# Kernel optimization log

Hardware: AMD Instinct MI355X
Metric: run time of the kernel (lower is better)

## Reference

```python
import jax, jax.numpy as jnp
import numpy as np

D_MODEL = 768
N_HEADS = 12
D_HEAD = D_MODEL // N_HEADS

def setup_inputs() -> dict:
    key = jax.random.key(0)
    ks = jax.random.split(key, 5)
    B, T = 2, 4096
    x = jax.random.normal(ks[0], (B, T, D_MODEL), dtype=jnp.float32)
    s_in = 1.0 / np.sqrt(D_MODEL)
    W_qkv = jax.random.normal(ks[1], (D_MODEL, 3 * D_MODEL), dtype=jnp.float32) * s_in
    b_qkv = jnp.zeros((3 * D_MODEL,), dtype=jnp.float32)
    W_proj = jax.random.normal(ks[2], (D_MODEL, D_MODEL), dtype=jnp.float32) * s_in
    b_proj = jnp.zeros((D_MODEL,), dtype=jnp.float32)
    return {"x": x, "W_qkv": W_qkv, "b_qkv": b_qkv, "W_proj": W_proj, "b_proj": b_proj}

def reference(x, W_qkv, b_qkv, W_proj, b_proj):
    B, T, C = x.shape
    qkv = x @ W_qkv + b_qkv                      # [B,T,3C]
    q, k, v = jnp.split(qkv, 3, axis=-1)
    def heads(t):
        return t.reshape(B, T, N_HEADS, D_HEAD).transpose(0, 2, 1, 3)  # [B,H,T,d]
    q, k, v = heads(q), heads(k), heads(v)
    scale = 1.0 / np.sqrt(D_HEAD)
    att = jnp.einsum('bhqd,bhkd->bhqk', q, k) * scale  # [B,H,T,T]
    causal = jnp.tril(jnp.ones((T, T), dtype=bool))
    att = jnp.where(causal[None, None], att, -jnp.inf)
    att = jax.nn.softmax(att, axis=-1)
    y = jnp.einsum('bhqk,bhkd->bhqd', att, v)          # [B,H,T,d]
    y = y.transpose(0, 2, 1, 3).reshape(B, T, C)
    return y @ W_proj + b_proj
```

## Files before the change

### kernel.cpp

```cpp
#include <hip/hip_runtime.h>
#include <hip/hip_bf16.h>

typedef __bf16 bf16_t;
typedef bf16_t bf16x8 __attribute__((ext_vector_type(8)));
typedef float  f32x4  __attribute__((ext_vector_type(4)));

#define TSEQ   4096
#define NBATCH 2
#define DMODEL 768
#define NHEADS 12
#define DHEAD  64
#define NTOK   (NBATCH*TSEQ)
#define NQKV   (3*DMODEL)

#define QSCALE 0.18033688011112042f
#define SMAX 24.0f

__device__ __forceinline__ f32x4 mfma16(bf16x8 a, bf16x8 b, f32x4 c) {
  return __builtin_amdgcn_mfma_f32_16x16x32_bf16(a, b, c, 0, 0, 0);
}

__device__ __forceinline__ void glds16(const bf16_t* g, bf16_t* l) {
  __builtin_amdgcn_global_load_lds(
      (const __attribute__((address_space(1))) void*)g,
      (__attribute__((address_space(3))) void*)l, 16, 0, 0);
}

__global__ void k_cvt(const float* __restrict__ in, bf16_t* __restrict__ out, int n) {
  int i = blockIdx.x * blockDim.x + threadIdx.x;
  if (i < n) out[i] = (bf16_t)in[i];
}

__global__ __launch_bounds__(256) void k_transpose_cvt(
    const float* __restrict__ in, bf16_t* __restrict__ out, int R, int C) {
  __shared__ bf16_t tile[64][66];
  const int c0 = blockIdx.x * 64, r0 = blockIdx.y * 64;
  const int tid = threadIdx.x;
  const int r = tid >> 2, cb = (tid & 3) * 16;
  const float* ip = in + (long)(r0 + r) * C + c0 + cb;
#pragma unroll
  for (int k = 0; k < 16; k += 4) {
    float4 v = *(const float4*)(ip + k);
    tile[r][cb + k + 0] = (bf16_t)v.x;
    tile[r][cb + k + 1] = (bf16_t)v.y;
    tile[r][cb + k + 2] = (bf16_t)v.z;
    tile[r][cb + k + 3] = (bf16_t)v.w;
  }
  __syncthreads();
  const int c = tid >> 2, rb = (tid & 3) * 16;
  bf16_t* op = out + (long)(c0 + c) * R + r0 + rb;
  bf16x8 v0, v1;
#pragma unroll
  for (int i = 0; i < 8; ++i) { v0[i] = tile[rb + i][c]; v1[i] = tile[rb + 8 + i][c]; }
  *(bf16x8*)(op) = v0;
  *(bf16x8*)(op + 8) = v1;
}

__device__ __forceinline__ void gemm_core(
    const bf16_t* __restrict__ A, const bf16_t* __restrict__ Bt,
    int m0, int n0, bf16_t* As, bf16_t* Bs, f32x4 acc[2][8]) {
  const int tid  = threadIdx.x;
  const int wave = tid >> 6;
  const int lane = tid & 63;
  const int quad = lane >> 4;
  const int l16  = lane & 15;
  const int srow = lane >> 2;
  const int scol = (lane & 3) * 8;

  const bf16_t* a0 = A + (long)(m0 + wave * 16 + srow) * DMODEL + scol;
  const bf16_t* b0 = Bt + (long)(n0 + wave * 16 + srow) * DMODEL + scol;

  glds16(a0,               As + wave * 16 * 32);
  glds16(a0 + 64 * DMODEL, As + (64 + wave * 16) * 32);
  glds16(b0,               Bs + wave * 16 * 32);
  glds16(b0 + 64 * DMODEL, Bs + (64 + wave * 16) * 32);
  __syncthreads();

  for (int ks = 0; ks < DMODEL / 32; ++ks) {
    const int p = ks & 1;
    if (ks + 1 < DMODEL / 32) {
      const int k1 = (ks + 1) * 32;
      bf16_t* Asx = (p ? As : As + 128 * 32);
      bf16_t* Bsx = (p ? Bs : Bs + 128 * 32);
      glds16(a0 + k1,               Asx + wave * 16 * 32);
      glds16(a0 + 64 * DMODEL + k1, Asx + (64 + wave * 16) * 32);
      glds16(b0 + k1,               Bsx + wave * 16 * 32);
      glds16(b0 + 64 * DMODEL + k1, Bsx + (64 + wave * 16) * 32);
    }
    const bf16_t* Ap = As + p * (128 * 32);
    const bf16_t* Bp = Bs + p * (128 * 32);

    bf16x8 af0 = *(const bf16x8*)(Ap + (wave * 32 + l16) * 32 + quad * 8);
    bf16x8 af1 = *(const bf16x8*)(Ap + (wave * 32 + 16 + l16) * 32 + quad * 8);
#pragma unroll
    for (int nt = 0; nt < 8; ++nt) {
      bf16x8 bfm = *(const bf16x8*)(Bp + (nt * 16 + l16) * 32 + quad * 8);
      acc[0][nt] = mfma16(af0, bfm, acc[0][nt]);
      acc[1][nt] = mfma16(af1, bfm, acc[1][nt]);
    }
    __syncthreads();
  }
}

__global__ __launch_bounds__(256) void k_gemm_qkv(
    const bf16_t* __restrict__ A, const bf16_t* __restrict__ Bt,
    const float* __restrict__ bias,
    bf16_t* __restrict__ Qo, bf16_t* __restrict__ Ko, bf16_t* __restrict__ Vo) {
  __shared__ __align__(16) bf16_t As[2 * 128 * 32];
  __shared__ __align__(16) bf16_t Bs[2 * 128 * 32];
  const int wave = threadIdx.x >> 6;
  const int lane = threadIdx.x & 63;
  const int quad = lane >> 4;
  const int l16  = lane & 15;
  const int m0 = blockIdx.x * 128;
  const int n0 = blockIdx.y * 128;

  f32x4 acc[2][8] = {};
  gemm_core(A, Bt, m0, n0, As, Bs, acc);

#pragma unroll
  for (int s = 0; s < 2; ++s)
#pragma unroll
    for (int nt = 0; nt < 8; ++nt) {
      const int n = n0 + nt * 16 + l16;
      const float bv = bias[n];
#pragma unroll
      for (int j = 0; j < 4; ++j) {
        const int m = m0 + wave * 32 + s * 16 + quad * 4 + j;
        const int b = m >> 12;
        const int t = m & 4095;
        const float v = acc[s][nt][j] + bv;
        if (n < DMODEL) {
          const int h = n >> 6, d = n & 63;
          Qo[(((long)(b * NHEADS + h) * TSEQ + t) << 6) + d] = (bf16_t)(v * QSCALE);
        } else if (n < 2 * DMODEL) {
          const int n2 = n - DMODEL, h = n2 >> 6, d = n2 & 63;
          Ko[(((long)(b * NHEADS + h) * TSEQ + t) << 6) + d] = (bf16_t)v;
        } else {
          const int n2 = n - 2 * DMODEL, h = n2 >> 6, d = n2 & 63;
          Vo[(((long)(b * NHEADS + h) * TSEQ + t) << 6) + d] = (bf16_t)v;
        }
      }
    }
}

__global__ __launch_bounds__(256) void k_gemm_proj(
    const bf16_t* __restrict__ A, const bf16_t* __restrict__ Bt,
    const float* __restrict__ bias, float* __restrict__ out) {
  __shared__ __align__(16) bf16_t As[2 * 128 * 32];
  __shared__ __align__(16) bf16_t Bs[2 * 128 * 32];
  const int wave = threadIdx.x >> 6;
  const int lane = threadIdx.x & 63;
  const int quad = lane >> 4;
  const int l16  = lane & 15;
  const int m0 = blockIdx.x * 128;
  const int n0 = blockIdx.y * 128;

  f32x4 acc[2][8] = {};
  gemm_core(A, Bt, m0, n0, As, Bs, acc);

#pragma unroll
  for (int s = 0; s < 2; ++s)
#pragma unroll
    for (int nt = 0; nt < 8; ++nt) {
      const int n = n0 + nt * 16 + l16;
      const float bv = bias[n];
#pragma unroll
      for (int j = 0; j < 4; ++j) {
        const int m = m0 + wave * 32 + s * 16 + quad * 4 + j;
        out[(long)m * DMODEL + n] = acc[s][nt][j] + bv;
      }
    }
}

__global__ __launch_bounds__(256) void k_vtrans(
    const bf16_t* __restrict__ V, bf16_t* __restrict__ Vt) {
  __shared__ bf16_t tile[64][72];
  const int tid = threadIdx.x;
  const int bh = blockIdx.y;
  const int t0 = blockIdx.x * 64;
  const bf16_t* Vh = V + ((long)bh * TSEQ << 6);
  bf16_t* VtH = Vt + (long)bh * DHEAD * TSEQ;

#pragma unroll
  for (int p = 0; p < 2; ++p) {
    const int t = p * 32 + (tid >> 3);
    const int d0 = (tid & 7) * 8;
    *(bf16x8*)&tile[t][d0] = *(const bf16x8*)(Vh + ((long)(t0 + t) << 6) + d0);
  }
  __syncthreads();
#pragma unroll
  for (int p = 0; p < 2; ++p) {
    const int d = p * 32 + (tid >> 3);
    const int tt = (tid & 7) * 8;
    bf16x8 v;
#pragma unroll
    for (int i = 0; i < 8; ++i) v[i] = tile[tt + i][d];
    *(bf16x8*)(VtH + (long)d * TSEQ + t0 + tt) = v;
  }
}

__global__ __launch_bounds__(256, 2) void k_attn(
    const bf16_t* __restrict__ Q, const bf16_t* __restrict__ K,
    const bf16_t* __restrict__ Vt,
    bf16_t* __restrict__ P0, bf16_t* __restrict__ P1,
    float* __restrict__ L0, float* __restrict__ L1) {
  __shared__ __align__(16) bf16_t kbuf[2][64 * 64];
  __shared__ __align__(16) bf16_t vbuf[2][64 * 64];
  const int wave = threadIdx.x >> 6;
  const int lane = threadIdx.x & 63;
  const int quad = lane >> 4;
  const int l16  = lane & 15;
  const int bh = blockIdx.x;
  const int qt = 15 - (blockIdx.y >> 1);
  const int sp = blockIdx.y & 1;
  const int nch = 4 * qt + 4, half = 2 * qt + 2;
  const int c0 = sp ? half : 0;
  const int niter = sp ? (nch - half) : half;
  bf16_t* Pp = sp ? P1 : P0;
  float*  Lp = sp ? L1 : L0;

  const bf16_t* Qh = Q + ((long)bh * TSEQ << 6);
  const bf16_t* Kh = K + ((long)bh * TSEQ << 6);
  const bf16_t* Vh = Vt + (long)bh * DHEAD * TSEQ;

  const int qbase = qt * 256 + wave * 64;

  bf16x8 qf[4][2];
#pragma unroll
  for (int s = 0; s < 4; ++s) {
    const bf16_t* qrow = Qh + ((long)(qbase + s * 16 + l16) << 6);
    qf[s][0] = *(const bf16x8*)(qrow + quad * 8);
    qf[s][1] = *(const bf16x8*)(qrow + 32 + quad * 8);
  }

  f32x4 acc[4][4] = {};
  f32x4 accL[4] = {};
  bf16x8 ones;
#pragma unroll
  for (int i = 0; i < 8; ++i) ones[i] = (bf16_t)1.0f;

  const int kperm = ((l16 >> 2) << 3) + (l16 & 3);
  const int swl = l16 & 7;
  const int srow = lane >> 3;
  const int cV = (lane & 7) ^ (srow & 7);
  const int cK0 = (lane & 7) ^ (srow & 3);
  const int cK1 = cK0 ^ 4;
  const int r0a = wave * 16, r0b = wave * 16 + 8;

  {
    const int k00 = c0 << 6;
    glds16(Kh + ((long)(k00 + r0a + srow) << 6) + cK0 * 8, &kbuf[0][r0a * 64]);
    glds16(Kh + ((long)(k00 + r0b + srow) << 6) + cK1 * 8, &kbuf[0][r0b * 64]);
    glds16(Vh + (long)(r0a + srow) * TSEQ + k00 + cV * 8,  &vbuf[0][r0a * 64]);
    glds16(Vh + (long)(r0b + srow) * TSEQ + k00 + cV * 8,  &vbuf[0][r0b * 64]);
  }
  __syncthreads();

  for (int ci = 0; ci < niter; ++ci) {
    const int p = ci & 1;
    const int k0 = (c0 + ci) << 6;
    if (ci + 1 < niter) {
      const int k1 = k0 + 64;
      glds16(Kh + ((long)(k1 + r0a + srow) << 6) + cK0 * 8, &kbuf[1 - p][r0a * 64]);
      glds16(Kh + ((long)(k1 + r0b + srow) << 6) + cK1 * 8, &kbuf[1 - p][r0b * 64]);
      glds16(Vh + (long)(r0a + srow) * TSEQ + k1 + cV * 8,  &vbuf[1 - p][r0a * 64]);
      glds16(Vh + (long)(r0b + srow) * TSEQ + k1 + cV * 8,  &vbuf[1 - p][r0b * 64]);
    }
    const bf16_t* kb = kbuf[p];
    const bf16_t* vb = vbuf[p];

#pragma unroll
    for (int g = 0; g < 2; ++g) {
      f32x4 st[4][2];
#pragma unroll
      for (int t = 0; t < 2; ++t) {
        const int row = g * 32 + t * 4 + kperm;
        bf16x8 kf0 = *(const bf16x8*)(kb + row * 64 + ((quad ^ swl) << 3));
        bf16x8 kf1 = *(const bf16x8*)(kb + row * 64 + (((quad + 4) ^ swl) << 3));
#pragma unroll
        for (int s = 0; s < 4; ++s) {
          f32x4 z = {};
          z = mfma16(kf0, qf[s][0], z);
          st[s][t] = mfma16(kf1, qf[s][1], z);
        }
      }
      if (k0 + g * 32 + 31 > qbase) {
#pragma unroll
        for (int s = 0; s < 4; ++s) {
          const int qS = qbase + s * 16 + l16;
#pragma unroll
          for (int t = 0; t < 2; ++t) {
            const int kbase = k0 + g * 32 + quad * 8 + t * 4;
#pragma unroll
            for (int j = 0; j < 4; ++j)
              if (kbase + j > qS) st[s][t][j] = -1e30f;
          }
        }
      }
      bf16x8 pf[4];
#pragma unroll
      for (int s = 0; s < 4; ++s) {
#pragma unroll
        for (int t = 0; t < 2; ++t)
#pragma unroll
          for (int j = 0; j < 4; ++j)
            pf[s][t * 4 + j] = (bf16_t)__builtin_amdgcn_exp2f(st[s][t][j] - SMAX);
        accL[s] = mfma16(ones, pf[s], accL[s]);
      }
#pragma unroll
      for (int dt = 0; dt < 4; ++dt) {
        const int row = dt * 16 + l16;
        bf16x8 vf = *(const bf16x8*)(vb + row * 64 + ((((g << 2) + quad) ^ swl) << 3));
#pragma unroll
        for (int s = 0; s < 4; ++s)
          acc[s][dt] = mfma16(vf, pf[s], acc[s][dt]);
      }
    }
    __syncthreads();
  }

#pragma unroll
  for (int s = 0; s < 4; ++s) {
    const int qS = qbase + s * 16 + l16;
    bf16_t* prow = Pp + (((long)bh * TSEQ + qS) << 6);
#pragma unroll
    for (int dt = 0; dt < 4; ++dt)
#pragma unroll
      for (int j = 0; j < 4; ++j)
        prow[dt * 16 + quad * 4 + j] = (bf16_t)acc[s][dt][j];
    if (quad == 0) Lp[(long)bh * TSEQ + qS] = accL[s][0];
  }
}

__global__ __launch_bounds__(128) void k_combine(
    const bf16_t* __restrict__ P0, const bf16_t* __restrict__ P1,
    const float* __restrict__ L0, const float* __restrict__ L1,
    bf16_t* __restrict__ Y) {
  const int row = blockIdx.x;
  const int tid = threadIdx.x;
  if (tid < 96) {
    const int b = row >> 12, q = row & 4095;
    const int h = tid >> 3, d0 = (tid & 7) * 8;
    const long bhq = (long)(b * NHEADS + h) * TSEQ + q;
    const long pidx = (bhq << 6) + d0;
    bf16x8 o0 = *(const bf16x8*)(P0 + pidx);
    bf16x8 o1 = *(const bf16x8*)(P1 + pidx);
    const float inv = 1.f / (L0[bhq] + L1[bhq]);
    bf16x8 r;
#pragma unroll
    for (int i = 0; i < 8; ++i) r[i] = (bf16_t)(((float)o0[i] + (float)o1[i]) * inv);
    *(bf16x8*)(Y + (long)row * DMODEL + tid * 8) = r;
  }
}

extern "C" void kernel_launch(void* const* d_in, const int* in_sizes, int n_in,
                              void* d_out, int out_size, void* d_ws, size_t ws_size,
                              hipStream_t stream) {
  (void)in_sizes; (void)n_in; (void)out_size; (void)ws_size;
  const float* x     = (const float*)d_in[0];
  const float* Wqkv  = (const float*)d_in[1];
  const float* bqkv  = (const float*)d_in[2];
  const float* Wproj = (const float*)d_in[3];
  const float* bproj = (const float*)d_in[4];
  float* out = (float*)d_out;

  char* ws = (char*)d_ws;
  bf16_t* Xb      = (bf16_t*)ws; ws += (long)NTOK * DMODEL * 2;
  bf16_t* wqkv_t  = (bf16_t*)ws; ws += (long)NQKV * DMODEL * 2;
  bf16_t* wproj_t = (bf16_t*)ws; ws += (long)DMODEL * DMODEL * 2;
  bf16_t* Qb      = (bf16_t*)ws; ws += (long)NTOK * DMODEL * 2;
  bf16_t* Kb      = (bf16_t*)ws; ws += (long)NTOK * DMODEL * 2;
  bf16_t* Vtb     = (bf16_t*)ws; ws += (long)NTOK * DMODEL * 2;
  bf16_t* Sb      = (bf16_t*)ws; ws += (long)NTOK * DMODEL * 2;
  bf16_t* P1b     = (bf16_t*)ws; ws += (long)NTOK * DMODEL * 2;
  float*  L0b     = (float*)ws;  ws += (long)NHEADS * NBATCH * TSEQ * 4;
  float*  L1b     = (float*)ws;  ws += (long)NHEADS * NBATCH * TSEQ * 4;
  bf16_t* P0b     = Xb;

  int n1 = NTOK * DMODEL;
  k_cvt<<<(n1 + 255) / 256, 256, 0, stream>>>(x, Xb, n1);
  k_transpose_cvt<<<dim3(NQKV / 64, DMODEL / 64), 256, 0, stream>>>(Wqkv, wqkv_t, DMODEL, NQKV);
  k_transpose_cvt<<<dim3(DMODEL / 64, DMODEL / 64), 256, 0, stream>>>(Wproj, wproj_t, DMODEL, DMODEL);

  k_gemm_qkv<<<dim3(NTOK / 128, NQKV / 128), 256, 0, stream>>>(Xb, wqkv_t, bqkv, Qb, Kb, Sb);
  k_vtrans<<<dim3(TSEQ / 64, NBATCH * NHEADS), 256, 0, stream>>>(Sb, Vtb);
  k_attn<<<dim3(NBATCH * NHEADS, 32), 256, 0, stream>>>(Qb, Kb, Vtb, P0b, P1b, L0b, L1b);
  k_combine<<<NTOK, 128, 0, stream>>>(P0b, P1b, L0b, L1b, Sb);
  k_gemm_proj<<<dim3(NTOK / 128, DMODEL / 128), 256, 0, stream>>>(Sb, wproj_t, bproj, out);
}
```

Before: 253.8 us.

## Fuse V transpose into QKV GEMM epilogue and compute softmax row sums with VALU

The QKV GEMM epilogue now writes V directly in the transposed [bh, d, t] layout with 4-wide vector stores, so the separate V-transpose kernel and its round trip through memory are removed. In the attention kernel, the row-sum MFMA against a ones vector is replaced by VALU accumulation plus cross-lane shuffles at the end. The SMAX offset is folded into the accumulator's initial value, and the K-fragment loads are hoisted. Occupancy is raised to 3 blocks per SM via launch bounds, which risks register spills.

Measured after the change: 353.2 us. 39.1% more time.

```diff
diff --git a/kernel.cpp b/kernel.cpp
--- a/kernel.cpp
+++ b/kernel.cpp
@@ -2,6 +2,7 @@
 #include <hip/hip_bf16.h>
 
 typedef __bf16 bf16_t;
+typedef bf16_t bf16x4 __attribute__((ext_vector_type(4)));
 typedef bf16_t bf16x8 __attribute__((ext_vector_type(8)));
 typedef float  f32x4  __attribute__((ext_vector_type(4)));
 
@@ -105,7 +106,7 @@
 __global__ __launch_bounds__(256) void k_gemm_qkv(
     const bf16_t* __restrict__ A, const bf16_t* __restrict__ Bt,
     const float* __restrict__ bias,
-    bf16_t* __restrict__ Qo, bf16_t* __restrict__ Ko, bf16_t* __restrict__ Vo) {
+    bf16_t* __restrict__ Qo, bf16_t* __restrict__ Ko, bf16_t* __restrict__ Vt) {
   __shared__ __align__(16) bf16_t As[2 * 128 * 32];
   __shared__ __align__(16) bf16_t Bs[2 * 128 * 32];
   const int wave = threadIdx.x >> 6;
@@ -124,22 +125,27 @@
     for (int nt = 0; nt < 8; ++nt) {
       const int n = n0 + nt * 16 + l16;
       const float bv = bias[n];
-#pragma unroll
-      for (int j = 0; j < 4; ++j) {
-        const int m = m0 + wave * 32 + s * 16 + quad * 4 + j;
-        const int b = m >> 12;
-        const int t = m & 4095;
-        const float v = acc[s][nt][j] + bv;
-        if (n < DMODEL) {
-          const int h = n >> 6, d = n & 63;
-          Qo[(((long)(b * NHEADS + h) * TSEQ + t) << 6) + d] = (bf16_t)(v * QSCALE);
-        } else if (n < 2 * DMODEL) {
-          const int n2 = n - DMODEL, h = n2 >> 6, d = n2 & 63;
-          Ko[(((long)(b * NHEADS + h) * TSEQ + t) << 6) + d] = (bf16_t)v;
-        } else {
-          const int n2 = n - 2 * DMODEL, h = n2 >> 6, d = n2 & 63;
-          Vo[(((long)(b * NHEADS + h) * TSEQ + t) << 6) + d] = (bf16_t)v;
-        }
+      const int mb = m0 + wave * 32 + s * 16 + quad * 4;
+      const int b = mb >> 12;
+      const int t = mb & 4095;
+      if (n < DMODEL) {
+        const int h = n >> 6, d = n & 63;
+        bf16_t* qp = Qo + (((long)(b * NHEADS + h) * TSEQ + t) << 6) + d;
+#pragma unroll
+        for (int j = 0; j < 4; ++j)
+          qp[(long)j << 6] = (bf16_t)((acc[s][nt][j] + bv) * QSCALE);
+      } else if (n < 2 * DMODEL) {
+        const int n2 = n - DMODEL, h = n2 >> 6, d = n2 & 63;
+        bf16_t* kp = Ko + (((long)(b * NHEADS + h) * TSEQ + t) << 6) + d;
+#pragma unroll
+        for (int j = 0; j < 4; ++j)
+          kp[(long)j << 6] = (bf16_t)(acc[s][nt][j] + bv);
+      } else {
+        const int n2 = n - 2 * DMODEL, h = n2 >> 6, d = n2 & 63;
+        bf16x4 v;
+#pragma unroll
+        for (int j = 0; j < 4; ++j) v[j] = (bf16_t)(acc[s][nt][j] + bv);
+        *(bf16x4*)(Vt + ((long)(b * NHEADS + h) * DHEAD + d) * TSEQ + t) = v;
       }
     }
 }
@@ -173,34 +179,7 @@
     }
 }
 
-__global__ __launch_bounds__(256) void k_vtrans(
-    const bf16_t* __restrict__ V, bf16_t* __restrict__ Vt) {
-  __shared__ bf16_t tile[64][72];
-  const int tid = threadIdx.x;
-  const int bh = blockIdx.y;
-  const int t0 = blockIdx.x * 64;
-  const bf16_t* Vh = V + ((long)bh * TSEQ << 6);
-  bf16_t* VtH = Vt + (long)bh * DHEAD * TSEQ;
-
-#pragma unroll
-  for (int p = 0; p < 2; ++p) {
-    const int t = p * 32 + (tid >> 3);
-    const int d0 = (tid & 7) * 8;
-    *(bf16x8*)&tile[t][d0] = *(const bf16x8*)(Vh + ((long)(t0 + t) << 6) + d0);
-  }
-  __syncthreads();
-#pragma unroll
-  for (int p = 0; p < 2; ++p) {
-    const int d = p * 32 + (tid >> 3);
-    const int tt = (tid & 7) * 8;
-    bf16x8 v;
-#pragma unroll
-    for (int i = 0; i < 8; ++i) v[i] = tile[tt + i][d];
-    *(bf16x8*)(VtH + (long)d * TSEQ + t0 + tt) = v;
-  }
-}
-
-__global__ __launch_bounds__(256, 2) void k_attn(
+__global__ __launch_bounds__(256, 3) void k_attn(
     const bf16_t* __restrict__ Q, const bf16_t* __restrict__ K,
     const bf16_t* __restrict__ Vt,
     bf16_t* __restrict__ P0, bf16_t* __restrict__ P1,
@@ -214,9 +193,9 @@
   const int bh = blockIdx.x;
   const int qt = 15 - (blockIdx.y >> 1);
   const int sp = blockIdx.y & 1;
-  const int nch = 4 * qt + 4, half = 2 * qt + 2;
+  const int half = 2 * qt + 2;
   const int c0 = sp ? half : 0;
-  const int niter = sp ? (nch - half) : half;
+  const int niter = half;
   bf16_t* Pp = sp ? P1 : P0;
   float*  Lp = sp ? L1 : L0;
 
@@ -235,10 +214,8 @@
   }
 
   f32x4 acc[4][4] = {};
-  f32x4 accL[4] = {};
-  bf16x8 ones;
-#pragma unroll
-  for (int i = 0; i < 8; ++i) ones[i] = (bf16_t)1.0f;
+  float lS[4] = {0.f, 0.f, 0.f, 0.f};
+  const f32x4 minit = {-SMAX, -SMAX, -SMAX, -SMAX};
 
   const int kperm = ((l16 >> 2) << 3) + (l16 & 3);
   const int swl = l16 & 7;
@@ -272,41 +249,41 @@
 
 #pragma unroll
     for (int g = 0; g < 2; ++g) {
-      f32x4 st[4][2];
-#pragma unroll
-      for (int t = 0; t < 2; ++t) {
-        const int row = g * 32 + t * 4 + kperm;
-        bf16x8 kf0 = *(const bf16x8*)(kb + row * 64 + ((quad ^ swl) << 3));
-        bf16x8 kf1 = *(const bf16x8*)(kb + row * 64 + (((quad + 4) ^ swl) << 3));
-#pragma unroll
-        for (int s = 0; s < 4; ++s) {
-          f32x4 z = {};
-          z = mfma16(kf0, qf[s][0], z);
-          st[s][t] = mfma16(kf1, qf[s][1], z);
-        }
-      }
-      if (k0 + g * 32 + 31 > qbase) {
-#pragma unroll
-        for (int s = 0; s < 4; ++s) {
+      const int rw0 = (g * 32 + kperm) * 64;
+      const int rw1 = (g * 32 + 4 + kperm) * 64;
+      bf16x8 kf00 = *(const bf16x8*)(kb + rw0 + ((quad ^ swl) << 3));
+      bf16x8 kf01 = *(const bf16x8*)(kb + rw0 + (((quad + 4) ^ swl) << 3));
+      bf16x8 kf10 = *(const bf16x8*)(kb + rw1 + ((quad ^ swl) << 3));
+      bf16x8 kf11 = *(const bf16x8*)(kb + rw1 + (((quad + 4) ^ swl) << 3));
+      const bool domask = (k0 + g * 32 + 31 > qbase);
+
+      bf16x8 pf[4];
+#pragma unroll
+      for (int s = 0; s < 4; ++s) {
+        f32x4 st0 = minit, st1 = minit;
+        st0 = mfma16(kf00, qf[s][0], st0);
+        st0 = mfma16(kf01, qf[s][1], st0);
+        st1 = mfma16(kf10, qf[s][0], st1);
+        st1 = mfma16(kf11, qf[s][1], st1);
+        if (domask) {
           const int qS = qbase + s * 16 + l16;
-#pragma unroll
-          for (int t = 0; t < 2; ++t) {
-            const int kbase = k0 + g * 32 + quad * 8 + t * 4;
-#pragma unroll
-            for (int j = 0; j < 4; ++j)
-              if (kbase + j > qS) st[s][t][j] = -1e30f;
+          const int kb0 = k0 + g * 32 + quad * 8;
+#pragma unroll
+          for (int j = 0; j < 4; ++j) {
+            if (kb0 + j > qS)     st0[j] = -1e30f;
+            if (kb0 + 4 + j > qS) st1[j] = -1e30f;
           }
         }
-      }
-      bf16x8 pf[4];
-#pragma unroll
-      for (int s = 0; s < 4; ++s) {
-#pragma unroll
-        for (int t = 0; t < 2; ++t)
-#pragma unroll
-          for (int j = 0; j < 4; ++j)
-            pf[s][t * 4 + j] = (bf16_t)__builtin_amdgcn_exp2f(st[s][t][j] - SMAX);
-        accL[s] = mfma16(ones, pf[s], accL[s]);
+        float rs = 0.f;
+#pragma unroll
+        for (int j = 0; j < 4; ++j) {
+          float e0 = __builtin_amdgcn_exp2f(st0[j]);
+          float e1 = __builtin_amdgcn_exp2f(st1[j]);
+          rs += e0 + e1;
+          pf[s][j]     = (bf16_t)e0;
+          pf[s][4 + j] = (bf16_t)e1;
+        }
+        lS[s] += rs;
       }
 #pragma unroll
       for (int dt = 0; dt < 4; ++dt) {
@@ -322,6 +299,11 @@
 
 #pragma unroll
   for (int s = 0; s < 4; ++s) {
+    lS[s] += __shfl_xor(lS[s], 16);
+    lS[s] += __shfl_xor(lS[s], 32);
+  }
+#pragma unroll
+  for (int s = 0; s < 4; ++s) {
     const int qS = qbase + s * 16 + l16;
     bf16_t* prow = Pp + (((long)bh * TSEQ + qS) << 6);
 #pragma unroll
@@ -329,7 +311,7 @@
 #pragma unroll
       for (int j = 0; j < 4; ++j)
         prow[dt * 16 + quad * 4 + j] = (bf16_t)acc[s][dt][j];
-    if (quad == 0) Lp[(long)bh * TSEQ + qS] = accL[s][0];
+    if (quad == 0) Lp[(long)bh * TSEQ + qS] = lS[s];
   }
 }
 
@@ -383,8 +365,7 @@
   k_transpose_cvt<<<dim3(NQKV / 64, DMODEL / 64), 256, 0, stream>>>(Wqkv, wqkv_t, DMODEL, NQKV);
   k_transpose_cvt<<<dim3(DMODEL / 64, DMODEL / 64), 256, 0, stream>>>(Wproj, wproj_t, DMODEL, DMODEL);
 
-  k_gemm_qkv<<<dim3(NTOK / 128, NQKV / 128), 256, 0, stream>>>(Xb, wqkv_t, bqkv, Qb, Kb, Sb);
-  k_vtrans<<<dim3(TSEQ / 64, NBATCH * NHEADS), 256, 0, stream>>>(Sb, Vtb);
+  k_gemm_qkv<<<dim3(NTOK / 128, NQKV / 128), 256, 0, stream>>>(Xb, wqkv_t, bqkv, Qb, Kb, Vtb);
   k_attn<<<dim3(NBATCH * NHEADS, 32), 256, 0, stream>>>(Qb, Kb, Vtb, P0b, P1b, L0b, L1b);
   k_combine<<<NTOK, 128, 0, stream>>>(P0b, P1b, L0b, L1b, Sb);
   k_gemm_proj<<<dim3(NTOK / 128, DMODEL / 128), 256, 0, stream>>>(Sb, wproj_t, bproj, out);
```
